# Performance work log

Hardware: AMD Instinct MI355X
Metric: run time of the kernel (lower is better)

The kernel has to match this reference:

```python
import jax, jax.numpy as jnp
import numpy as np

NUM_HEADS = 12

def setup_inputs() -> dict:
    key = jax.random.key(0)
    k1, k2, k3 = jax.random.split(key, 3)
    B, T, H = 2, 2048, 768
    x = jax.random.normal(k1, (B, T, H), dtype=jnp.float32)
    attn_mask = jnp.ones((B, T), dtype=jnp.int32)
    Wqkv = jax.random.normal(k2, (H, 3 * H), dtype=jnp.float32) * 0.02
    bqkv = jnp.zeros((3 * H,), dtype=jnp.float32)
    Wproj = jax.random.normal(k3, (H, H), dtype=jnp.float32) * 0.02
    bproj = jnp.zeros((H,), dtype=jnp.float32)
    return {"x": x, "attn_mask": attn_mask, "Wqkv": Wqkv, "bqkv": bqkv,
            "Wproj": Wproj, "bproj": bproj}

def reference(x, attn_mask, Wqkv, bqkv, Wproj, bproj):
    B, T, H = x.shape
    nh = NUM_HEADS
    hd = H // nh
    qkv = x @ Wqkv + bqkv                      # [B,T,3H]
    q, k, v = jnp.split(qkv, 3, axis=-1)
    # [B,T,H] -> [B,nh,T,hd]
    def heads(t):
        return t.reshape(B, T, nh, hd).transpose(0, 2, 1, 3)
    q, k, v = heads(q), heads(k), heads(v)
    scores = jnp.einsum('bhqd,bhkd->bhqk', q, k) / jnp.sqrt(jnp.float32(hd))
    causal = jnp.tril(jnp.ones((T, T), dtype=bool))          # allowed positions
    key_ok = attn_mask.astype(bool)[:, None, None, :]        # [B,1,1,T]
    allowed = causal[None, None] & key_ok
    scores = jnp.where(allowed, scores, -jnp.inf)
    weights = jax.nn.softmax(scores, axis=-1)                # dropout=0 (eval)
    out = jnp.einsum('bhqk,bhkd->bhqd', weights, v)
    out = out.transpose(0, 2, 1, 3).reshape(B, T, H)
    return out @ Wproj + bproj
```

## Files before the change

kernel.cpp:

```cpp
#include <hip/hip_runtime.h>
#include <stdint.h>

typedef unsigned short u16;
typedef unsigned int   u32;
typedef unsigned char  u8;
typedef __attribute__((ext_vector_type(8))) short short8;
typedef __attribute__((ext_vector_type(4))) float f32x4;
typedef __attribute__((ext_vector_type(4))) unsigned short u16x4;

#define DEV static __device__ __forceinline__

static constexpr int Bc = 2, Tc = 2048, Hc = 768, NH = 12, HD = 64;
static constexpr int BTc = Bc * Tc;
static constexpr int N3 = 3 * Hc;
static constexpr int NBH = Bc * NH;
static constexpr int NITEMS = 32 * NBH;
static constexpr float QSCALE = 0.125f * 1.44269504088896f;
static constexpr float MRINIT = -1.0e38f;
static constexpr float SMASK  = -3.0e38f;

DEV u16 f2bf(float f) {
  u32 u = __float_as_uint(f);
  u32 r = (u + 0x7fffu + ((u >> 16) & 1u)) >> 16;
  return (u16)r;
}

DEV float fexp2(float x) {
#if __has_builtin(__builtin_amdgcn_exp2f)
  return __builtin_amdgcn_exp2f(x);
#else
  return exp2f(x);
#endif
}

DEV u32 cvtpk_bf16(float lo, float hi) {
  u32 r;
  asm("v_cvt_pk_bf16_f32 %0, %1, %2" : "=v"(r) : "v"(lo), "v"(hi));
  return r;
}

DEV void gl_lds16(const u16* g, u16* l) {
  __builtin_amdgcn_global_load_lds(
      (const __attribute__((address_space(1))) u32*)g,
      (__attribute__((address_space(3))) u32*)l, 16, 0, 0);
}

#define MFMA(a, b, c) __builtin_amdgcn_mfma_f32_16x16x32_bf16((a), (b), (c), 0, 0, 0)

__global__ void k_cvt(const float4* __restrict__ in, uint4* __restrict__ out, int n8,
                      const int* __restrict__ mask, u8* __restrict__ flags,
                      u32* __restrict__ ctr) {
  if (blockIdx.x == 0 && threadIdx.x < 64) {
    int t = threadIdx.x;
    if (t == 0) *ctr = 0;
    int b = t >> 5, kb = t & 31;
    const int* m = mask + b * Tc + kb * 64;
    int all = 1;
    for (int i = 0; i < 64; ++i) all &= (m[i] != 0);
    flags[b * 32 + kb] = (u8)all;
  }
  int i = blockIdx.x * 256 + threadIdx.x;
  if (i >= n8) return;
  float4 a = in[2 * i], b = in[2 * i + 1];
  uint4 o;
  o.x = f2bf(a.x) | ((u32)f2bf(a.y) << 16);
  o.y = f2bf(a.z) | ((u32)f2bf(a.w) << 16);
  o.z = f2bf(b.x) | ((u32)f2bf(b.y) << 16);
  o.w = f2bf(b.z) | ((u32)f2bf(b.w) << 16);
  out[i] = o;
}

__global__ __launch_bounds__(256) void k_transpose_w(const float* __restrict__ in,
                                                     u16* __restrict__ out, int R, int C) {
  __shared__ u16 tile[64][65];
  int c0 = blockIdx.x * 64, r0 = blockIdx.y * 64;
  int tx = threadIdx.x, ty = threadIdx.y;
  for (int i = ty; i < 64; i += 4)
    tile[i][tx] = f2bf(in[(size_t)(r0 + i) * C + c0 + tx]);
  __syncthreads();
  for (int i = ty; i < 64; i += 4)
    out[(size_t)(c0 + i) * R + r0 + tx] = tile[tx][i];
}

template <int EPI>
__global__ __launch_bounds__(256) void k_gemm(const u16* __restrict__ A,
                                              const u16* __restrict__ BTm,
                                              const float* __restrict__ bias,
                                              u16* __restrict__ oQ, u16* __restrict__ oK,
                                              u16* __restrict__ oV, float* __restrict__ oF,
                                              int M, int N, int K) {
  __shared__ u16 As[128 * 32];
  __shared__ u16 Bs[128 * 32];
  const int tid = threadIdx.x;
  const int lane = tid & 63, wave = tid >> 6;
  const int wr = wave >> 1, wc = wave & 1;
  const int row0 = blockIdx.y * 128, col0 = blockIdx.x * 128;

  f32x4 acc[4][4];
#pragma unroll
  for (int m = 0; m < 4; ++m)
#pragma unroll
    for (int n = 0; n < 4; ++n) acc[m][n] = (f32x4)(0.f);

  const int srow = lane >> 2;
  const int sg = lane & 3;
  const int sf = (lane >> 3) & 3;
  const int kfetch = ((sg ^ sf) * 8);

  const int r16 = lane & 15;
  const int g = lane >> 4;
  const int fr = (r16 >> 1) & 3;
  const int koff = ((g ^ fr) * 8);

  for (int k0 = 0; k0 < K; k0 += 32) {
    if (k0) __syncthreads();
#pragma unroll
    for (int p = 0; p < 2; ++p) {
      int seg = wave * 2 + p;
      int row = seg * 16 + srow;
      gl_lds16(A + (size_t)(row0 + row) * K + k0 + kfetch, &As[seg * 512 + lane * 8]);
      gl_lds16(BTm + (size_t)(col0 + row) * K + k0 + kfetch, &Bs[seg * 512 + lane * 8]);
    }
    __syncthreads();
    short8 af[4], bf[4];
#pragma unroll
    for (int m = 0; m < 4; ++m)
      af[m] = *(const short8*)&As[(wr * 64 + m * 16 + r16) * 32 + koff];
#pragma unroll
    for (int n = 0; n < 4; ++n)
      bf[n] = *(const short8*)&Bs[(wc * 64 + n * 16 + r16) * 32 + koff];
#pragma unroll
    for (int m = 0; m < 4; ++m)
#pragma unroll
      for (int n = 0; n < 4; ++n)
        acc[m][n] = MFMA(af[m], bf[n], acc[m][n]);
  }

#pragma unroll
  for (int m = 0; m < 4; ++m) {
    int rowg = row0 + wr * 64 + m * 16 + g * 4;
#pragma unroll
    for (int n = 0; n < 4; ++n) {
      int colg = col0 + wc * 64 + n * 16 + r16;
      float bv = bias[colg];
      if constexpr (EPI == 0) {
        int which = colg / Hc;
        int hc = colg - which * Hc;
        int h = hc >> 6, d = hc & 63;
        int b = rowg >> 11, t0 = rowg & 2047;
        if (which == 2) {
          u16x4 pk;
#pragma unroll
          for (int r = 0; r < 4; ++r) pk[r] = f2bf(acc[m][n][r] + bv);
          *(u16x4*)&oV[((size_t)(b * NH + h) * HD + d) * Tc + t0] = pk;
        } else {
#pragma unroll
          for (int r = 0; r < 4; ++r) {
            float v = acc[m][n][r] + bv;
            size_t dst = ((size_t)(b * NH + h) * Tc + t0 + r) * HD + d;
            if (which == 0) oQ[dst] = f2bf(v * QSCALE);
            else            oK[dst] = f2bf(v);
          }
        }
      } else {
#pragma unroll
        for (int r = 0; r < 4; ++r)
          oF[(size_t)(rowg + r) * Hc + colg] = acc[m][n][r] + bv;
      }
    }
  }
}

__global__ __launch_bounds__(512, 4) void k_attn(const u16* __restrict__ Qh,
                                                 const u16* __restrict__ Kh,
                                                 const u16* __restrict__ VT,
                                                 const int* __restrict__ mask,
                                                 const u8* __restrict__ flags,
                                                 u16* __restrict__ O,
                                                 u32* __restrict__ ctr) {
  __shared__ u16 Ks[4][4096];
  __shared__ u16 Vs[4][4096];
  __shared__ u16 Ps[8][512];
  __shared__ int s_item;
  const int tid = threadIdx.x, lane = tid & 63, wave = tid >> 6;
  const int qgrp = wave >> 1;
  const int kh = wave & 1;
  const int r16 = lane & 15, g = lane >> 4;
  const int r7 = r16 & 7;
  const int skey = lane >> 3;
  const int sgr = lane & 7;
  const int sgd = ((sgr ^ skey) * 8);

  const int off0 = r16 * 64 + ((g ^ r7) * 8);
  const int off1 = r16 * 64 + (((4 + g) ^ r7) * 8);
  const int offv = kh ? off1 : off0;
  const int prd = r16 * 16 + ((g ^ (r16 & 3)) << 2);

  for (;;) {
    if (tid == 0) s_item = (int)atomicAdd(ctr, 1u);
    __syncthreads();
    const int item = s_item;
    if (item >= NITEMS) break;
    const int qt = 31 - item / NBH;
    const int bh = item % NBH;
    const int b = bh / NH, h = bh - b * NH;
    const int q0 = qt * 64;
    const int nt = qt + 1;
    const int qg = q0 + qgrp * 16 + r16;
    const int* mrow = mask + b * Tc;
    const u8* frow = flags + b * 32;

    const u16* qbase = Qh + ((size_t)bh * Tc + qg) * HD;
    const short8 qf0 = *(const short8*)(qbase + g * 8);
    const short8 qf1 = *(const short8*)(qbase + 32 + g * 8);

    f32x4 acc[4];
#pragma unroll
    for (int n = 0; n < 4; ++n) acc[n] = (f32x4)(0.f);
    float mrun = MRINIT, lrun = 0.f;

    {
      int rloc = wave * 8 + skey;
      gl_lds16(Kh + ((size_t)bh * Tc + rloc) * HD + sgd, &Ks[0][wave * 512 + lane * 8]);
      gl_lds16(VT + ((size_t)bh * HD + rloc) * Tc + sgd, &Vs[0][wave * 512 + lane * 8]);
      if (nt > 1) {
        gl_lds16(Kh + ((size_t)bh * Tc + 64 + rloc) * HD + sgd, &Ks[1][wave * 512 + lane * 8]);
        gl_lds16(VT + ((size_t)bh * HD + rloc) * Tc + 64 + sgd, &Vs[1][wave * 512 + lane * 8]);
      }
    }

    for (int t = 0; t < nt; ++t) {
      const int kb = t * 64;
      const int rem = nt - 1 - t;

      if (rem >= 2) {
        const int kb2 = kb + 128;
        const int sp = (t + 2) & 3;
        int rloc = wave * 8 + skey;
        gl_lds16(Kh + ((size_t)bh * Tc + kb2 + rloc) * HD + sgd,
                 &Ks[sp][wave * 512 + lane * 8]);
        gl_lds16(VT + ((size_t)bh * HD + rloc) * Tc + kb2 + sgd,
                 &Vs[sp][wave * 512 + lane * 8]);
      }

      if (rem >= 2)      asm volatile("s_waitcnt vmcnt(4)" ::: "memory");
      else if (rem == 1) asm volatile("s_waitcnt vmcnt(2)" ::: "memory");
      else               asm volatile("s_waitcnt vmcnt(0)" ::: "memory");
      __builtin_amdgcn_sched_barrier(0);
      __builtin_amdgcn_s_barrier();
      __builtin_amdgcn_sched_barrier(0);

      const u16* Kc = &Ks[t & 3][0];
      const u16* Vc = &Vs[t & 3][0];

      f32x4 s[2];
      __builtin_amdgcn_s_setprio(1);
#pragma unroll
      for (int np = 0; np < 2; ++np) {
        const int ng = 2 * kh + np;
        short8 kf0 = *(const short8*)&Kc[ng * 1024 + off0];
        short8 kf1 = *(const short8*)&Kc[ng * 1024 + off1];
        f32x4 z = (f32x4)(0.f);
        z = MFMA(kf0, qf0, z);
        z = MFMA(kf1, qf1, z);
        s[np] = z;
      }
      __builtin_amdgcn_s_setprio(0);

      const bool diag = (t == nt - 1);
      if (diag || !frow[t]) {
        const int fl = frow[t];
#pragma unroll
        for (int np = 0; np < 2; ++np)
#pragma unroll
          for (int r = 0; r < 4; ++r) {
            int keyg = kb + 16 * (2 * kh + np) + 4 * g + r;
            bool ok = fl ? true : (mrow[keyg] != 0);
            if (diag) ok = ok && (keyg <= qg);
            if (!ok) s[np][r] = SMASK;
          }
      }

      float lm;
      {
        float m0 = fmaxf(fmaxf(s[0][0], s[0][1]), fmaxf(s[0][2], s[0][3]));
        float m1 = fmaxf(fmaxf(s[1][0], s[1][1]), fmaxf(s[1][2], s[1][3]));
        lm = fmaxf(m0, m1);
      }
      if (!__all(lm <= mrun + 8.0f)) {
        float rm = fmaxf(lm, __shfl_xor(lm, 16));
        rm = fmaxf(rm, __shfl_xor(rm, 32));
        float nm = fmaxf(mrun, rm);
        float alpha = fexp2(mrun - nm);
        mrun = nm;
        lrun *= alpha;
#pragma unroll
        for (int r = 0; r < 4; ++r) {
          float ar = __shfl(alpha, g * 4 + r);
          acc[0][r] *= ar;
          acc[1][r] *= ar;
          acc[2][r] *= ar;
          acc[3][r] *= ar;
        }
      }
      float rs = 0.f;
#pragma unroll
      for (int np = 0; np < 2; ++np)
#pragma unroll
        for (int r = 0; r < 4; ++r) {
          float p = fexp2(s[np][r] - mrun);
          s[np][r] = p;
          rs += p;
        }
      lrun += rs;

      u32* pw = (u32*)&Ps[wave][0];
#pragma unroll
      for (int np = 0; np < 2; ++np) {
        u32 lo = cvtpk_bf16(s[np][0], s[np][1]);
        u32 hi = cvtpk_bf16(s[np][2], s[np][3]);
        int kg = 2 * np + (g >> 1);
        int idx = r16 * 16 + ((kg ^ (r16 & 3)) << 2) + 2 * (g & 1);
        *(uint2*)&pw[idx] = make_uint2(lo, hi);
      }
      short8 pa = *(const short8*)&pw[prd];

      __builtin_amdgcn_s_setprio(1);
#pragma unroll
      for (int n = 0; n < 4; ++n) {
        short8 vf = *(const short8*)&Vc[n * 1024 + offv];
        acc[n] = MFMA(pa, vf, acc[n]);
      }
      __builtin_amdgcn_s_setprio(0);
      __builtin_amdgcn_sched_barrier(0);
    }

    float lt = lrun + __shfl_xor(lrun, 16);
    lt += __shfl_xor(lt, 32);

    __syncthreads();
    float* ab = (float*)&Ks[0][0] + qgrp * 1024;
    float* ml = (float*)&Ps[0][0];
    if (kh == 1) {
#pragma unroll
      for (int n = 0; n < 4; ++n)
#pragma unroll
        for (int r = 0; r < 4; ++r)
          ab[(4 * g + r) * 64 + 16 * n + r16] = acc[n][r];
      if (g == 0) {
        ml[qgrp * 32 + r16 * 2]     = mrun;
        ml[qgrp * 32 + r16 * 2 + 1] = lt;
      }
    }
    __syncthreads();
    if (kh == 0) {
#pragma unroll
      for (int r = 0; r < 4; ++r) {
        int q = 4 * g + r;
        float mA = __shfl(mrun, q);
        float lA = __shfl(lt, q);
        float mB = ml[qgrp * 32 + q * 2];
        float lB = ml[qgrp * 32 + q * 2 + 1];
        float ms = fmaxf(mA, mB);
        float cA = fexp2(mA - ms);
        float cB = fexp2(mB - ms);
        float linv = 1.0f / (lA * cA + lB * cB);
        int qr = q0 + qgrp * 16 + q;
        u16* orow = O + ((size_t)(b * Tc + qr)) * Hc + h * 64;
#pragma unroll
        for (int n = 0; n < 4; ++n) {
          float v = (acc[n][r] * cA + ab[q * 64 + 16 * n + r16] * cB) * linv;
          orow[n * 16 + r16] = f2bf(v);
        }
      }
    }
  }
}

extern "C" void kernel_launch(void* const* d_in, const int* in_sizes, int n_in,
                              void* d_out, int out_size, void* d_ws, size_t ws_size,
                              hipStream_t stream) {
  const float* x = (const float*)d_in[0];
  const int* mask = (const int*)d_in[1];
  const float* Wqkv = (const float*)d_in[2];
  const float* bqkv = (const float*)d_in[3];
  const float* Wproj = (const float*)d_in[4];
  const float* bproj = (const float*)d_in[5];
  float* out = (float*)d_out;

  char* ws = (char*)d_ws;
  size_t off = 0;
  auto alloc = [&](size_t bytes) {
    char* p = ws + off;
    off += (bytes + 255) & ~(size_t)255;
    return p;
  };
  u16* xb     = (u16*)alloc((size_t)BTc * Hc * 2);
  u16* WqkvT  = (u16*)alloc((size_t)N3 * Hc * 2);
  u16* WprojT = (u16*)alloc((size_t)Hc * Hc * 2);
  u16* Qh     = (u16*)alloc((size_t)BTc * Hc * 2);
  u16* Kh     = (u16*)alloc((size_t)BTc * Hc * 2);
  u16* VT     = (u16*)alloc((size_t)BTc * Hc * 2);
  u32* ctr    = (u32*)alloc(256);
  u8*  flags  = (u8*)alloc(256);
  u16* Ob     = xb;

  int n8 = BTc * Hc / 8;
  k_cvt<<<(n8 + 255) / 256, 256, 0, stream>>>((const float4*)x, (uint4*)xb, n8,
                                              mask, flags, ctr);
  k_transpose_w<<<dim3(N3 / 64, Hc / 64), dim3(64, 4), 0, stream>>>(Wqkv, WqkvT, Hc, N3);
  k_transpose_w<<<dim3(Hc / 64, Hc / 64), dim3(64, 4), 0, stream>>>(Wproj, WprojT, Hc, Hc);
  k_gemm<0><<<dim3(N3 / 128, BTc / 128), 256, 0, stream>>>(xb, WqkvT, bqkv, Qh, Kh, VT,
                                                           nullptr, BTc, N3, Hc);
  k_attn<<<dim3(512), 512, 0, stream>>>(Qh, Kh, VT, mask, flags, Ob, ctr);
  k_gemm<1><<<dim3(Hc / 128, BTc / 128), 256, 0, stream>>>(Ob, WprojT, bproj, nullptr,
                                                           nullptr, nullptr, out, BTc, Hc, Hc);
}
```

Before: 107.1 us.

## Process 128-key tiles per attention iteration and merge weight transpose launches

Measured after the change: 100.3 us. -6.4%, faster.

```diff
diff --git a/kernel.cpp b/kernel.cpp
--- a/kernel.cpp
+++ b/kernel.cpp
@@ -70,10 +70,18 @@
   out[i] = o;
 }
 
-__global__ __launch_bounds__(256) void k_transpose_w(const float* __restrict__ in,
-                                                     u16* __restrict__ out, int R, int C) {
+__global__ __launch_bounds__(256) void k_transpose_w2(const float* __restrict__ Wqkv,
+                                                      const float* __restrict__ Wproj,
+                                                      u16* __restrict__ WqkvT,
+                                                      u16* __restrict__ WprojT) {
   __shared__ u16 tile[64][65];
-  int c0 = blockIdx.x * 64, r0 = blockIdx.y * 64;
+  int y = blockIdx.y, x = blockIdx.x;
+  const float* in; u16* out; int R, C, r0, c0;
+  if (y < 12) { in = Wqkv; out = WqkvT; R = Hc; C = N3; r0 = y * 64; c0 = x * 64; }
+  else {
+    if (x >= 12) return;
+    in = Wproj; out = WprojT; R = Hc; C = Hc; r0 = (y - 12) * 64; c0 = x * 64;
+  }
   int tx = threadIdx.x, ty = threadIdx.y;
   for (int i = ty; i < 64; i += 4)
     tile[i][tx] = f2bf(in[(size_t)(r0 + i) * C + c0 + tx]);
@@ -178,10 +186,11 @@
                                                  const u8* __restrict__ flags,
                                                  u16* __restrict__ O,
                                                  u32* __restrict__ ctr) {
-  __shared__ u16 Ks[4][4096];
-  __shared__ u16 Vs[4][4096];
-  __shared__ u16 Ps[8][512];
-  __shared__ int s_item;
+  __shared__ u16 Ks[2][8192];
+  __shared__ u16 Vs[2][8192];
+  __shared__ u16 Ps[8][1024];
+  int* s_item = (int*)&Ps[1][0];
+  float* ml = (float*)&Ps[0][0];
   const int tid = threadIdx.x, lane = tid & 63, wave = tid >> 6;
   const int qgrp = wave >> 1;
   const int kh = wave & 1;
@@ -193,19 +202,19 @@
 
   const int off0 = r16 * 64 + ((g ^ r7) * 8);
   const int off1 = r16 * 64 + (((4 + g) ^ r7) * 8);
-  const int offv = kh ? off1 : off0;
-  const int prd = r16 * 16 + ((g ^ (r16 & 3)) << 2);
+  const int vo0 = r16 * 128 + (kh * 8 + (g ^ r7)) * 8;
+  const int vo1 = r16 * 128 + (kh * 8 + ((4 + g) ^ r7)) * 8;
 
   for (;;) {
-    if (tid == 0) s_item = (int)atomicAdd(ctr, 1u);
+    if (tid == 0) *s_item = (int)atomicAdd(ctr, 1u);
     __syncthreads();
-    const int item = s_item;
+    const int item = *s_item;
     if (item >= NITEMS) break;
     const int qt = 31 - item / NBH;
     const int bh = item % NBH;
     const int b = bh / NH, h = bh - b * NH;
     const int q0 = qt * 64;
-    const int nt = qt + 1;
+    const int nt = qt / 2 + 1;
     const int qg = q0 + qgrp * 16 + r16;
     const int* mrow = mask + b * Tc;
     const u8* frow = flags + b * 32;
@@ -219,119 +228,126 @@
     for (int n = 0; n < 4; ++n) acc[n] = (f32x4)(0.f);
     float mrun = MRINIT, lrun = 0.f;
 
-    {
-      int rloc = wave * 8 + skey;
-      gl_lds16(Kh + ((size_t)bh * Tc + rloc) * HD + sgd, &Ks[0][wave * 512 + lane * 8]);
-      gl_lds16(VT + ((size_t)bh * HD + rloc) * Tc + sgd, &Vs[0][wave * 512 + lane * 8]);
-      if (nt > 1) {
-        gl_lds16(Kh + ((size_t)bh * Tc + 64 + rloc) * HD + sgd, &Ks[1][wave * 512 + lane * 8]);
-        gl_lds16(VT + ((size_t)bh * HD + rloc) * Tc + 64 + sgd, &Vs[1][wave * 512 + lane * 8]);
-      }
-    }
+    auto stage = [&](int slot, int kb) {
+#pragma unroll
+      for (int p = 0; p < 2; ++p) {
+        int seg = 2 * wave + p;
+        int rloc = 8 * seg + skey;
+        gl_lds16(Kh + ((size_t)bh * Tc + kb + rloc) * HD + sgd,
+                 &Ks[slot][seg * 512 + lane * 8]);
+      }
+#pragma unroll
+      for (int p = 0; p < 2; ++p) {
+        int dloc = 8 * wave + 4 * p + g;
+        int vsg = (((r16 & 8) | ((r16 & 7) ^ (dloc & 7)))) * 8;
+        gl_lds16(VT + ((size_t)bh * HD + dloc) * Tc + kb + vsg,
+                 &Vs[slot][wave * 1024 + p * 512 + lane * 8]);
+      }
+    };
+
+    stage(0, 0);
 
     for (int t = 0; t < nt; ++t) {
-      const int kb = t * 64;
-      const int rem = nt - 1 - t;
-
-      if (rem >= 2) {
-        const int kb2 = kb + 128;
-        const int sp = (t + 2) & 3;
-        int rloc = wave * 8 + skey;
-        gl_lds16(Kh + ((size_t)bh * Tc + kb2 + rloc) * HD + sgd,
-                 &Ks[sp][wave * 512 + lane * 8]);
-        gl_lds16(VT + ((size_t)bh * HD + rloc) * Tc + kb2 + sgd,
-                 &Vs[sp][wave * 512 + lane * 8]);
-      }
-
-      if (rem >= 2)      asm volatile("s_waitcnt vmcnt(4)" ::: "memory");
-      else if (rem == 1) asm volatile("s_waitcnt vmcnt(2)" ::: "memory");
-      else               asm volatile("s_waitcnt vmcnt(0)" ::: "memory");
+      const int kb = t * 128;
+
+      asm volatile("s_waitcnt vmcnt(0)" ::: "memory");
       __builtin_amdgcn_sched_barrier(0);
       __builtin_amdgcn_s_barrier();
       __builtin_amdgcn_sched_barrier(0);
 
-      const u16* Kc = &Ks[t & 3][0];
-      const u16* Vc = &Vs[t & 3][0];
-
-      f32x4 s[2];
-      __builtin_amdgcn_s_setprio(1);
-#pragma unroll
-      for (int np = 0; np < 2; ++np) {
-        const int ng = 2 * kh + np;
-        short8 kf0 = *(const short8*)&Kc[ng * 1024 + off0];
-        short8 kf1 = *(const short8*)&Kc[ng * 1024 + off1];
-        f32x4 z = (f32x4)(0.f);
-        z = MFMA(kf0, qf0, z);
-        z = MFMA(kf1, qf1, z);
-        s[np] = z;
-      }
-      __builtin_amdgcn_s_setprio(0);
-
-      const bool diag = (t == nt - 1);
-      if (diag || !frow[t]) {
-        const int fl = frow[t];
-#pragma unroll
-        for (int np = 0; np < 2; ++np)
+      if (t + 1 < nt) stage((t + 1) & 1, kb + 128);
+
+      const u16* Kc = &Ks[t & 1][0];
+      const u16* Vc = &Vs[t & 1][0];
+
+      const int kbw = kb + 64 * kh;
+      const bool dead = (kbw > q0 + 63);
+      if (!dead) {
+        f32x4 s[4];
+        __builtin_amdgcn_s_setprio(1);
+#pragma unroll
+        for (int nn = 0; nn < 4; ++nn) {
+          const int ng = 4 * kh + nn;
+          short8 kf0 = *(const short8*)&Kc[ng * 1024 + off0];
+          short8 kf1 = *(const short8*)&Kc[ng * 1024 + off1];
+          f32x4 z = (f32x4)(0.f);
+          z = MFMA(kf0, qf0, z);
+          z = MFMA(kf1, qf1, z);
+          s[nn] = z;
+        }
+        __builtin_amdgcn_s_setprio(0);
+
+        const bool diag = (kbw == q0);
+        if (diag || !frow[2 * t + kh]) {
+          const int fl = frow[2 * t + kh];
+#pragma unroll
+          for (int nn = 0; nn < 4; ++nn)
+#pragma unroll
+            for (int r = 0; r < 4; ++r) {
+              int keyg = kbw + 16 * nn + 4 * g + r;
+              bool ok = fl ? true : (mrow[keyg] != 0);
+              if (diag) ok = ok && (keyg <= qg);
+              if (!ok) s[nn][r] = SMASK;
+            }
+        }
+
+        float lm;
+        {
+          float m0 = fmaxf(fmaxf(s[0][0], s[0][1]), fmaxf(s[0][2], s[0][3]));
+          float m1 = fmaxf(fmaxf(s[1][0], s[1][1]), fmaxf(s[1][2], s[1][3]));
+          float m2 = fmaxf(fmaxf(s[2][0], s[2][1]), fmaxf(s[2][2], s[2][3]));
+          float m3 = fmaxf(fmaxf(s[3][0], s[3][1]), fmaxf(s[3][2], s[3][3]));
+          lm = fmaxf(fmaxf(m0, m1), fmaxf(m2, m3));
+        }
+        if (!__all(lm <= mrun + 8.0f)) {
+          float rm = fmaxf(lm, __shfl_xor(lm, 16));
+          rm = fmaxf(rm, __shfl_xor(rm, 32));
+          float nm = fmaxf(mrun, rm);
+          float alpha = fexp2(mrun - nm);
+          mrun = nm;
+          lrun *= alpha;
 #pragma unroll
           for (int r = 0; r < 4; ++r) {
-            int keyg = kb + 16 * (2 * kh + np) + 4 * g + r;
-            bool ok = fl ? true : (mrow[keyg] != 0);
-            if (diag) ok = ok && (keyg <= qg);
-            if (!ok) s[np][r] = SMASK;
+            float ar = __shfl(alpha, g * 4 + r);
+            acc[0][r] *= ar;
+            acc[1][r] *= ar;
+            acc[2][r] *= ar;
+            acc[3][r] *= ar;
           }
-      }
-
-      float lm;
-      {
-        float m0 = fmaxf(fmaxf(s[0][0], s[0][1]), fmaxf(s[0][2], s[0][3]));
-        float m1 = fmaxf(fmaxf(s[1][0], s[1][1]), fmaxf(s[1][2], s[1][3]));
-        lm = fmaxf(m0, m1);
-      }
-      if (!__all(lm <= mrun + 8.0f)) {
-        float rm = fmaxf(lm, __shfl_xor(lm, 16));
-        rm = fmaxf(rm, __shfl_xor(rm, 32));
-        float nm = fmaxf(mrun, rm);
-        float alpha = fexp2(mrun - nm);
-        mrun = nm;
-        lrun *= alpha;
-#pragma unroll
-        for (int r = 0; r < 4; ++r) {
-          float ar = __shfl(alpha, g * 4 + r);
-          acc[0][r] *= ar;
-          acc[1][r] *= ar;
-          acc[2][r] *= ar;
-          acc[3][r] *= ar;
-        }
-      }
-      float rs = 0.f;
-#pragma unroll
-      for (int np = 0; np < 2; ++np)
-#pragma unroll
-        for (int r = 0; r < 4; ++r) {
-          float p = fexp2(s[np][r] - mrun);
-          s[np][r] = p;
-          rs += p;
-        }
-      lrun += rs;
-
-      u32* pw = (u32*)&Ps[wave][0];
-#pragma unroll
-      for (int np = 0; np < 2; ++np) {
-        u32 lo = cvtpk_bf16(s[np][0], s[np][1]);
-        u32 hi = cvtpk_bf16(s[np][2], s[np][3]);
-        int kg = 2 * np + (g >> 1);
-        int idx = r16 * 16 + ((kg ^ (r16 & 3)) << 2) + 2 * (g & 1);
-        *(uint2*)&pw[idx] = make_uint2(lo, hi);
-      }
-      short8 pa = *(const short8*)&pw[prd];
-
-      __builtin_amdgcn_s_setprio(1);
-#pragma unroll
-      for (int n = 0; n < 4; ++n) {
-        short8 vf = *(const short8*)&Vc[n * 1024 + offv];
-        acc[n] = MFMA(pa, vf, acc[n]);
-      }
-      __builtin_amdgcn_s_setprio(0);
+        }
+        float rs = 0.f;
+#pragma unroll
+        for (int nn = 0; nn < 4; ++nn)
+#pragma unroll
+          for (int r = 0; r < 4; ++r) {
+            float p = fexp2(s[nn][r] - mrun);
+            s[nn][r] = p;
+            rs += p;
+          }
+        lrun += rs;
+
+        u32* pw = (u32*)&Ps[wave][0];
+#pragma unroll
+        for (int nn = 0; nn < 4; ++nn) {
+          u32 lo = cvtpk_bf16(s[nn][0], s[nn][1]);
+          u32 hi = cvtpk_bf16(s[nn][2], s[nn][3]);
+          int idx = r16 * 32 + (((2 * nn + (g >> 1)) ^ r7) << 2) + 2 * (g & 1);
+          *(uint2*)&pw[idx] = make_uint2(lo, hi);
+        }
+        const u16* pr = &Ps[wave][0];
+        short8 pa0 = *(const short8*)&pr[off0];
+        short8 pa1 = *(const short8*)&pr[off1];
+
+        __builtin_amdgcn_s_setprio(1);
+#pragma unroll
+        for (int n = 0; n < 4; ++n) {
+          short8 vf0 = *(const short8*)&Vc[n * 2048 + vo0];
+          short8 vf1 = *(const short8*)&Vc[n * 2048 + vo1];
+          acc[n] = MFMA(pa0, vf0, acc[n]);
+          acc[n] = MFMA(pa1, vf1, acc[n]);
+        }
+        __builtin_amdgcn_s_setprio(0);
+      }
       __builtin_amdgcn_sched_barrier(0);
     }
 
@@ -340,7 +356,6 @@
 
     __syncthreads();
     float* ab = (float*)&Ks[0][0] + qgrp * 1024;
-    float* ml = (float*)&Ps[0][0];
     if (kh == 1) {
 #pragma unroll
       for (int n = 0; n < 4; ++n)
@@ -408,8 +423,7 @@
   int n8 = BTc * Hc / 8;
   k_cvt<<<(n8 + 255) / 256, 256, 0, stream>>>((const float4*)x, (uint4*)xb, n8,
                                               mask, flags, ctr);
-  k_transpose_w<<<dim3(N3 / 64, Hc / 64), dim3(64, 4), 0, stream>>>(Wqkv, WqkvT, Hc, N3);
-  k_transpose_w<<<dim3(Hc / 64, Hc / 64), dim3(64, 4), 0, stream>>>(Wproj, WprojT, Hc, Hc);
+  k_transpose_w2<<<dim3(36, 24), dim3(64, 4), 0, stream>>>(Wqkv, Wproj, WqkvT, WprojT);
   k_gemm<0><<<dim3(N3 / 128, BTc / 128), 256, 0, stream>>>(xb, WqkvT, bqkv, Qh, Kh, VT,
                                                            nullptr, BTc, N3, Hc);
   k_attn<<<dim3(512), 512, 0, stream>>>(Qh, Kh, VT, mask, flags, Ob, ctr);
```

## Software-pipeline attention QK and softmax, keep P in registers, fuse weight transposes

Applied to the files above, without the earlier changes.

After: 103.6 us. 3.3% less time.

```diff
diff --git a/kernel.cpp b/kernel.cpp
--- a/kernel.cpp
+++ b/kernel.cpp
@@ -7,6 +7,7 @@
 typedef __attribute__((ext_vector_type(8))) short short8;
 typedef __attribute__((ext_vector_type(4))) float f32x4;
 typedef __attribute__((ext_vector_type(4))) unsigned short u16x4;
+typedef __attribute__((ext_vector_type(4))) unsigned int u32x4;
 
 #define DEV static __device__ __forceinline__
 
@@ -70,10 +71,18 @@
   out[i] = o;
 }
 
-__global__ __launch_bounds__(256) void k_transpose_w(const float* __restrict__ in,
-                                                     u16* __restrict__ out, int R, int C) {
+__global__ __launch_bounds__(256) void k_transpose_w2(const float* __restrict__ Wqkv,
+                                                      const float* __restrict__ Wproj,
+                                                      u16* __restrict__ WqkvT,
+                                                      u16* __restrict__ WprojT) {
   __shared__ u16 tile[64][65];
-  int c0 = blockIdx.x * 64, r0 = blockIdx.y * 64;
+  int y = blockIdx.y, x = blockIdx.x;
+  const float* in; u16* out; int R, C, r0, c0;
+  if (y < 12) { in = Wqkv; out = WqkvT; R = Hc; C = N3; r0 = y * 64; c0 = x * 64; }
+  else {
+    if (x >= 12) return;
+    in = Wproj; out = WprojT; R = Hc; C = Hc; r0 = (y - 12) * 64; c0 = x * 64;
+  }
   int tx = threadIdx.x, ty = threadIdx.y;
   for (int i = ty; i < 64; i += 4)
     tile[i][tx] = f2bf(in[(size_t)(r0 + i) * C + c0 + tx]);
@@ -149,10 +158,12 @@
         int h = hc >> 6, d = hc & 63;
         int b = rowg >> 11, t0 = rowg & 2047;
         if (which == 2) {
+          int o = t0 & 31;
+          int t0p = (t0 & ~31) | (((o >> 2) & 3) * 8 + ((o >> 4) & 1) * 4);
           u16x4 pk;
 #pragma unroll
           for (int r = 0; r < 4; ++r) pk[r] = f2bf(acc[m][n][r] + bv);
-          *(u16x4*)&oV[((size_t)(b * NH + h) * HD + d) * Tc + t0] = pk;
+          *(u16x4*)&oV[((size_t)(b * NH + h) * HD + d) * Tc + t0p] = pk;
         } else {
 #pragma unroll
           for (int r = 0; r < 4; ++r) {
@@ -180,7 +191,7 @@
                                                  u32* __restrict__ ctr) {
   __shared__ u16 Ks[4][4096];
   __shared__ u16 Vs[4][4096];
-  __shared__ u16 Ps[8][512];
+  __shared__ float mlb[128];
   __shared__ int s_item;
   const int tid = threadIdx.x, lane = tid & 63, wave = tid >> 6;
   const int qgrp = wave >> 1;
@@ -194,7 +205,6 @@
   const int off0 = r16 * 64 + ((g ^ r7) * 8);
   const int off1 = r16 * 64 + (((4 + g) ^ r7) * 8);
   const int offv = kh ? off1 : off0;
-  const int prd = r16 * 16 + ((g ^ (r16 & 3)) << 2);
 
   for (;;) {
     if (tid == 0) s_item = (int)atomicAdd(ctr, 1u);
@@ -219,74 +229,33 @@
     for (int n = 0; n < 4; ++n) acc[n] = (f32x4)(0.f);
     float mrun = MRINIT, lrun = 0.f;
 
-    {
+    const u16* kgb = Kh + (size_t)bh * Tc * HD;
+    const u16* vgb = VT + (size_t)bh * HD * Tc;
+
+    auto stage = [&](int slot, int kb) {
       int rloc = wave * 8 + skey;
-      gl_lds16(Kh + ((size_t)bh * Tc + rloc) * HD + sgd, &Ks[0][wave * 512 + lane * 8]);
-      gl_lds16(VT + ((size_t)bh * HD + rloc) * Tc + sgd, &Vs[0][wave * 512 + lane * 8]);
-      if (nt > 1) {
-        gl_lds16(Kh + ((size_t)bh * Tc + 64 + rloc) * HD + sgd, &Ks[1][wave * 512 + lane * 8]);
-        gl_lds16(VT + ((size_t)bh * HD + rloc) * Tc + 64 + sgd, &Vs[1][wave * 512 + lane * 8]);
-      }
-    }
-
-    for (int t = 0; t < nt; ++t) {
-      const int kb = t * 64;
-      const int rem = nt - 1 - t;
-
-      if (rem >= 2) {
-        const int kb2 = kb + 128;
-        const int sp = (t + 2) & 3;
-        int rloc = wave * 8 + skey;
-        gl_lds16(Kh + ((size_t)bh * Tc + kb2 + rloc) * HD + sgd,
-                 &Ks[sp][wave * 512 + lane * 8]);
-        gl_lds16(VT + ((size_t)bh * HD + rloc) * Tc + kb2 + sgd,
-                 &Vs[sp][wave * 512 + lane * 8]);
-      }
-
-      if (rem >= 2)      asm volatile("s_waitcnt vmcnt(4)" ::: "memory");
-      else if (rem == 1) asm volatile("s_waitcnt vmcnt(2)" ::: "memory");
-      else               asm volatile("s_waitcnt vmcnt(0)" ::: "memory");
-      __builtin_amdgcn_sched_barrier(0);
-      __builtin_amdgcn_s_barrier();
-      __builtin_amdgcn_sched_barrier(0);
-
-      const u16* Kc = &Ks[t & 3][0];
-      const u16* Vc = &Vs[t & 3][0];
-
-      f32x4 s[2];
-      __builtin_amdgcn_s_setprio(1);
-#pragma unroll
-      for (int np = 0; np < 2; ++np) {
-        const int ng = 2 * kh + np;
-        short8 kf0 = *(const short8*)&Kc[ng * 1024 + off0];
-        short8 kf1 = *(const short8*)&Kc[ng * 1024 + off1];
-        f32x4 z = (f32x4)(0.f);
-        z = MFMA(kf0, qf0, z);
-        z = MFMA(kf1, qf1, z);
-        s[np] = z;
-      }
-      __builtin_amdgcn_s_setprio(0);
-
-      const bool diag = (t == nt - 1);
-      if (diag || !frow[t]) {
-        const int fl = frow[t];
+      gl_lds16(kgb + (size_t)(kb + rloc) * HD + sgd, &Ks[slot][wave * 512 + lane * 8]);
+      gl_lds16(vgb + (size_t)rloc * Tc + kb + sgd, &Vs[slot][wave * 512 + lane * 8]);
+    };
+
+    f32x4 sP0, sP1;
+    auto process = [&](int u, f32x4 s0, f32x4 s1) {
+      const int kbw = 64 * u + 32 * kh;
+      const bool diag = (u == nt - 1);
+      if (diag || !frow[u]) {
+        const int fl = frow[u];
 #pragma unroll
         for (int np = 0; np < 2; ++np)
 #pragma unroll
           for (int r = 0; r < 4; ++r) {
-            int keyg = kb + 16 * (2 * kh + np) + 4 * g + r;
+            int keyg = kbw + 16 * np + 4 * g + r;
             bool ok = fl ? true : (mrow[keyg] != 0);
             if (diag) ok = ok && (keyg <= qg);
-            if (!ok) s[np][r] = SMASK;
+            if (!ok) { if (np == 0) s0[r] = SMASK; else s1[r] = SMASK; }
           }
       }
-
-      float lm;
-      {
-        float m0 = fmaxf(fmaxf(s[0][0], s[0][1]), fmaxf(s[0][2], s[0][3]));
-        float m1 = fmaxf(fmaxf(s[1][0], s[1][1]), fmaxf(s[1][2], s[1][3]));
-        lm = fmaxf(m0, m1);
-      }
+      float lm = fmaxf(fmaxf(fmaxf(s0[0], s0[1]), fmaxf(s0[2], s0[3])),
+                       fmaxf(fmaxf(s1[0], s1[1]), fmaxf(s1[2], s1[3])));
       if (!__all(lm <= mrun + 8.0f)) {
         float rm = fmaxf(lm, __shfl_xor(lm, 16));
         rm = fmaxf(rm, __shfl_xor(rm, 32));
@@ -297,34 +266,21 @@
 #pragma unroll
         for (int r = 0; r < 4; ++r) {
           float ar = __shfl(alpha, g * 4 + r);
-          acc[0][r] *= ar;
-          acc[1][r] *= ar;
-          acc[2][r] *= ar;
-          acc[3][r] *= ar;
+          acc[0][r] *= ar; acc[1][r] *= ar; acc[2][r] *= ar; acc[3][r] *= ar;
         }
       }
-      float rs = 0.f;
-#pragma unroll
-      for (int np = 0; np < 2; ++np)
-#pragma unroll
-        for (int r = 0; r < 4; ++r) {
-          float p = fexp2(s[np][r] - mrun);
-          s[np][r] = p;
-          rs += p;
-        }
-      lrun += rs;
-
-      u32* pw = (u32*)&Ps[wave][0];
-#pragma unroll
-      for (int np = 0; np < 2; ++np) {
-        u32 lo = cvtpk_bf16(s[np][0], s[np][1]);
-        u32 hi = cvtpk_bf16(s[np][2], s[np][3]);
-        int kg = 2 * np + (g >> 1);
-        int idx = r16 * 16 + ((kg ^ (r16 & 3)) << 2) + 2 * (g & 1);
-        *(uint2*)&pw[idx] = make_uint2(lo, hi);
-      }
-      short8 pa = *(const short8*)&pw[prd];
-
+      float p0[4], p1[4];
+#pragma unroll
+      for (int r = 0; r < 4; ++r) {
+        p0[r] = fexp2(s0[r] - mrun);
+        p1[r] = fexp2(s1[r] - mrun);
+      }
+      lrun += ((p0[0] + p0[1]) + (p0[2] + p0[3])) + ((p1[0] + p1[1]) + (p1[2] + p1[3]));
+      u32x4 PL;
+      PL[0] = cvtpk_bf16(p0[0], p0[1]); PL[1] = cvtpk_bf16(p0[2], p0[3]);
+      PL[2] = cvtpk_bf16(p1[0], p1[1]); PL[3] = cvtpk_bf16(p1[2], p1[3]);
+      short8 pa = __builtin_bit_cast(short8, PL);
+      const u16* Vc = &Vs[u & 3][0];
       __builtin_amdgcn_s_setprio(1);
 #pragma unroll
       for (int n = 0; n < 4; ++n) {
@@ -332,15 +288,51 @@
         acc[n] = MFMA(pa, vf, acc[n]);
       }
       __builtin_amdgcn_s_setprio(0);
+    };
+
+    stage(0, 0);
+    if (nt > 1) stage(1, 64);
+
+    for (int t = 0; t < nt; ++t) {
+      const int kb = t * 64;
+      const int rem = nt - 1 - t;
+
+      if (rem >= 1) asm volatile("s_waitcnt vmcnt(2)" ::: "memory");
+      else          asm volatile("s_waitcnt vmcnt(0)" ::: "memory");
       __builtin_amdgcn_sched_barrier(0);
+      __builtin_amdgcn_s_barrier();
+      __builtin_amdgcn_sched_barrier(0);
+
+      if (rem >= 2) stage((t + 2) & 3, kb + 128);
+
+      const u16* Kc = &Ks[t & 3][0];
+      f32x4 sN0, sN1;
+      __builtin_amdgcn_s_setprio(1);
+      {
+        const int ng = 2 * kh;
+        short8 kf0 = *(const short8*)&Kc[ng * 1024 + off0];
+        short8 kf1 = *(const short8*)&Kc[ng * 1024 + off1];
+        f32x4 z = (f32x4)(0.f);
+        z = MFMA(kf0, qf0, z); z = MFMA(kf1, qf1, z);
+        sN0 = z;
+        short8 kf2 = *(const short8*)&Kc[(ng + 1) * 1024 + off0];
+        short8 kf3 = *(const short8*)&Kc[(ng + 1) * 1024 + off1];
+        f32x4 w = (f32x4)(0.f);
+        w = MFMA(kf2, qf0, w); w = MFMA(kf3, qf1, w);
+        sN1 = w;
+      }
+      __builtin_amdgcn_s_setprio(0);
+
+      if (t > 0) process(t - 1, sP0, sP1);
+      sP0 = sN0; sP1 = sN1;
     }
+    process(nt - 1, sP0, sP1);
 
     float lt = lrun + __shfl_xor(lrun, 16);
     lt += __shfl_xor(lt, 32);
 
     __syncthreads();
     float* ab = (float*)&Ks[0][0] + qgrp * 1024;
-    float* ml = (float*)&Ps[0][0];
     if (kh == 1) {
 #pragma unroll
       for (int n = 0; n < 4; ++n)
@@ -348,8 +340,8 @@
         for (int r = 0; r < 4; ++r)
           ab[(4 * g + r) * 64 + 16 * n + r16] = acc[n][r];
       if (g == 0) {
-        ml[qgrp * 32 + r16 * 2]     = mrun;
-        ml[qgrp * 32 + r16 * 2 + 1] = lt;
+        mlb[qgrp * 32 + r16 * 2]     = mrun;
+        mlb[qgrp * 32 + r16 * 2 + 1] = lt;
       }
     }
     __syncthreads();
@@ -359,8 +351,8 @@
         int q = 4 * g + r;
         float mA = __shfl(mrun, q);
         float lA = __shfl(lt, q);
-        float mB = ml[qgrp * 32 + q * 2];
-        float lB = ml[qgrp * 32 + q * 2 + 1];
+        float mB = mlb[qgrp * 32 + q * 2];
+        float lB = mlb[qgrp * 32 + q * 2 + 1];
         float ms = fmaxf(mA, mB);
         float cA = fexp2(mA - ms);
         float cB = fexp2(mB - ms);
@@ -408,8 +400,7 @@
   int n8 = BTc * Hc / 8;
   k_cvt<<<(n8 + 255) / 256, 256, 0, stream>>>((const float4*)x, (uint4*)xb, n8,
                                               mask, flags, ctr);
-  k_transpose_w<<<dim3(N3 / 64, Hc / 64), dim3(64, 4), 0, stream>>>(Wqkv, WqkvT, Hc, N3);
-  k_transpose_w<<<dim3(Hc / 64, Hc / 64), dim3(64, 4), 0, stream>>>(Wproj, WprojT, Hc, Hc);
+  k_transpose_w2<<<dim3(36, 24), dim3(64, 4), 0, stream>>>(Wqkv, Wproj, WqkvT, WprojT);
   k_gemm<0><<<dim3(N3 / 128, BTc / 128), 256, 0, stream>>>(xb, WqkvT, bqkv, Qh, Kh, VT,
                                                            nullptr, BTc, N3, Hc);
   k_attn<<<dim3(512), 512, 0, stream>>>(Qh, Kh, VT, mask, flags, Ob, ctr);
```
